# Kernel tuning notes

Hardware: AMD Instinct MI355X
Metric: run time of the kernel (lower is better)

Reference implementation:

```python
import jax, jax.numpy as jnp
import numpy as np

B, S, H, E, V, OOV = 64, 400, 512, 256, 50000, 100

def setup_inputs() -> dict:
    key = jax.random.key(0)
    ks = jax.random.split(key, 32)
    p = lambda i, shape: jax.random.normal(ks[i], shape, jnp.float32) * 0.02
    emb = p(0, (V, E)).at[0].set(0.0)  # padding_idx=0
    return dict(
        summaries_in=jax.random.randint(ks[1], (B,), 1, V),
        h0=jax.random.normal(ks[2], (B, H), jnp.float32),
        c0=jax.random.normal(ks[3], (B, H), jnp.float32),
        encoder_out=jax.random.normal(ks[4], (B, S, 2 * H), jnp.float32),
        encoder_features=jax.random.normal(ks[5], (S * B, 2 * H), jnp.float32),
        encoder_mask=jnp.ones((S, B), jnp.float32),
        context=jax.random.normal(ks[6], (B, 2 * H), jnp.float32),
        coverage=jax.random.uniform(ks[7], (S, B), jnp.float32) * 0.01,
        texts_extended=jax.random.randint(ks[8], (S, B), 0, V + OOV),
        oov_size=OOV,
        emb=emb,
        W_feat=p(10, (2 * H, 2 * H)), b_feat=p(11, (2 * H,)),
        W_cov=p(12, (2 * H,)), b_cov=p(13, (2 * H,)),
        w_att=p(14, (2 * H,)), b_att=p(15, ()),
        W_ih=p(16, (4 * H, E)), W_hh=p(17, (4 * H, H)),
        b_ih=p(18, (4 * H,)), b_hh=p(19, (4 * H,)),
        W_ctx=p(20, (E, 2 * H + E)), b_ctx=p(21, (E,)),
        W_pg=p(22, (4 * H + E,)), b_pg=p(23, ()),
        W_o1=p(24, (H, 3 * H)), b_o1=p(25, (H,)),
        W_o2=p(26, (V, H)), b_o2=p(27, (V,)),
    )


def reference(summaries_in, h0, c0, encoder_out, encoder_features, encoder_mask,
              context, coverage, texts_extended, oov_size, emb,
              W_feat, b_feat, W_cov, b_cov, w_att, b_att,
              W_ih, W_hh, b_ih, b_hh, W_ctx, b_ctx, W_pg, b_pg,
              W_o1, b_o1, W_o2, b_o2):
    # embedding + context projection: [B, 2H+E] -> [B, E]
    x = emb[summaries_in]
    ctx_out = jnp.concatenate([context, x], axis=1) @ W_ctx.T + b_ctx
    # single LSTM step (torch gate order i, f, g, o)
    gates = ctx_out @ W_ih.T + b_ih + h0 @ W_hh.T + b_hh
    i, f, g, o = jnp.split(gates, 4, axis=1)
    c = jax.nn.sigmoid(f) * c0 + jax.nn.sigmoid(i) * jnp.tanh(g)
    h = jax.nn.sigmoid(o) * jnp.tanh(c)
    hidden_out = jnp.concatenate([h, c], axis=1)  # [B, 2H]
    # Bahdanau attention with coverage
    dec_feat = hidden_out @ W_feat.T + b_feat                 # [B, 2H]
    ef = encoder_features.reshape(S, B, 2 * H)                # [S, B, 2H]
    cov_feat = coverage[..., None] * W_cov + b_cov            # Linear(1, 2H)
    e = jnp.tanh(ef + dec_feat[None] + cov_feat) @ w_att + b_att  # [S, B]
    a = jax.nn.softmax(e, axis=0) * encoder_mask
    a = a / jnp.sum(a, axis=0, keepdims=True)                 # renormalize (Normalize(0))
    ctx_new = jnp.einsum('sb,bsd->bd', a, encoder_out)        # [B, 2H]
    coverage_next = coverage + a
    # pointer-generator mix
    gen_in = jnp.concatenate([ctx_new, hidden_out, ctx_out], axis=1)  # [B, 4H+E]
    p_gen = jax.nn.sigmoid(gen_in @ W_pg + b_pg)[:, None]             # [B, 1]
    logits = (jnp.concatenate([h, ctx_new], axis=1) @ W_o1.T + b_o1) @ W_o2.T + b_o2
    vocab_dist = p_gen * jax.nn.softmax(logits, axis=1)       # [B, V]
    attn_w = (1.0 - p_gen) * a.T                              # [B, S]
    vd = jnp.concatenate([vocab_dist, jnp.zeros((B, oov_size), vocab_dist.dtype)], axis=1)
    vd = vd.at[jnp.arange(B)[:, None], texts_extended.T].add(attn_w)  # scatter_add copy dist
    return vd, hidden_out, ctx_new, a, coverage_next
```

## Files before the change

### kernel.cpp

```cpp
#include <hip/hip_runtime.h>
#include <cmath>

#define B 64
#define S 400
#define H 512
#define E 256
#define V 50000
#define OOV 100
#define H2 1024
#define VDN (V + OOV)
#define NBLK_V 782
#define SC 25

typedef __attribute__((ext_vector_type(8))) short short8;
typedef __attribute__((ext_vector_type(4))) float f32x4;

__device__ __forceinline__ float wred_sum(float v) {
#pragma unroll
  for (int o = 32; o > 0; o >>= 1) v += __shfl_down(v, o, 64);
  return v;
}
__device__ __forceinline__ float wred_max(float v) {
#pragma unroll
  for (int o = 32; o > 0; o >>= 1) v = fmaxf(v, __shfl_down(v, o, 64));
  return v;
}
__device__ __forceinline__ short f2bf(float f) {
  return __builtin_bit_cast(short, (__bf16)f);
}
__device__ __forceinline__ float bf2f(unsigned short u) {
  unsigned x = (unsigned)u << 16;
  return __builtin_bit_cast(float, x);
}
__device__ __forceinline__ float ftanh(float x) {
  float e = __expf(2.f * x);
  return 1.f - 2.f * __builtin_amdgcn_rcpf(e + 1.f);
}
__device__ __forceinline__ float fsig(float x) {
  return __builtin_amdgcn_rcpf(1.f + __expf(-x));
}

__global__ __launch_bounds__(256) void k_pre(
    const float* __restrict__ b_ctx, const float* __restrict__ b_ih,
    const float* __restrict__ b_hh, const float* __restrict__ b_feat,
    const float* __restrict__ b_o1, const float* __restrict__ context,
    const float* __restrict__ emb, const int* __restrict__ sumin,
    const float* __restrict__ h0, float* __restrict__ ctxoutT4,
    float* __restrict__ gates, float* __restrict__ dfeat,
    float* __restrict__ innerT4, float* __restrict__ catT4,
    float* __restrict__ h0T4, float* __restrict__ Zb) {
  int idx = blockIdx.x * 256 + threadIdx.x;
  if (idx < 64) Zb[idx] = 0.f;
  if (idx < 16384) {
    int j = ((idx >> 8) << 2) + (idx & 3);
    ctxoutT4[idx] = b_ctx[j];
  } else if (idx < 16384 + 131072) {
    int i = idx - 16384;
    int j = i & 2047;
    gates[i] = b_ih[j] + b_hh[j];
  } else if (idx < 16384 + 131072 + 65536) {
    int i = idx - 16384 - 131072;
    dfeat[i] = b_feat[i & 1023];
  } else if (idx < 245760) {
    int i = idx - 16384 - 131072 - 65536;
    int j = ((i >> 8) << 2) + (i & 3);
    innerT4[i] = b_o1[j];
  } else if (idx < 245760 + 81920) {
    int i = idx - 245760;
    int e = i & 3, b = (i >> 2) & 63, q = i >> 8;
    int k = q * 4 + e;
    catT4[i] = (k < 1024) ? context[b * 1024 + k]
                          : emb[(size_t)sumin[b] * 256 + (k - 1024)];
  } else {
    int i = idx - 245760 - 81920;
    int e = i & 3, b = (i >> 2) & 63, q = i >> 8;
    h0T4[i] = h0[b * 512 + q * 4 + e];
  }
}

template <int R, int KC, int OUTMODE>
__global__ __launch_bounds__(256) void k_gemmsk(
    const float* __restrict__ A1, const float* __restrict__ W1, int ldw1, int s1,
    const float* __restrict__ A2, const float* __restrict__ W2, int ldw2,
    float* __restrict__ out, int ldout) {
  const int lane = threadIdx.x;
  const int w = threadIdx.y;
  const int j0 = blockIdx.x * (4 * R) + w * R;
  const float* A;
  const float* W;
  int ldw, kc0;
  if ((int)blockIdx.y < s1) {
    A = A1; W = W1; ldw = ldw1; kc0 = blockIdx.y * KC;
  } else {
    A = A2; W = W2; ldw = ldw2; kc0 = (blockIdx.y - s1) * KC;
  }
  float acc[R];
#pragma unroll
  for (int r = 0; r < R; ++r) acc[r] = 0.f;
  const float* ap = A + (size_t)kc0 * 256 + lane * 4;
  const float* wr[R];
#pragma unroll
  for (int r = 0; r < R; ++r) wr[r] = W + (size_t)(j0 + r) * ldw + kc0 * 4;
#pragma unroll 8
  for (int k4 = 0; k4 < KC; ++k4) {
    float4 av = *(const float4*)(ap + (size_t)k4 * 256);
#pragma unroll
    for (int r = 0; r < R; ++r) {
      float4 wv = *(const float4*)(wr[r] + k4 * 4);
      acc[r] += av.x * wv.x + av.y * wv.y + av.z * wv.z + av.w * wv.w;
    }
  }
#pragma unroll
  for (int r = 0; r < R; ++r) {
    int j = j0 + r;
    if constexpr (OUTMODE == 0)
      atomicAdd(&out[((size_t)(j >> 2) * 64 + lane) * 4 + (j & 3)], acc[r]);
    else
      atomicAdd(&out[(size_t)lane * ldout + j], acc[r]);
  }
}

__global__ __launch_bounds__(256) void k_lstm(const float* __restrict__ gates,
                                              const float* __restrict__ c0,
                                              float* __restrict__ hidden,
                                              float* __restrict__ hcT4) {
  int idx = blockIdx.x * 256 + threadIdx.x;
  int b = idx >> 9, u = idx & 511;
  float gi = gates[(size_t)b * 2048 + u];
  float gf = gates[(size_t)b * 2048 + 512 + u];
  float gg = gates[(size_t)b * 2048 + 1024 + u];
  float go = gates[(size_t)b * 2048 + 1536 + u];
  float c = fsig(gf) * c0[(size_t)b * 512 + u] + fsig(gi) * ftanh(gg);
  float h = fsig(go) * ftanh(c);
  hidden[(size_t)b * H2 + u] = h;
  hidden[(size_t)b * H2 + 512 + u] = c;
  hcT4[((u >> 2) * 64 + b) * 4 + (u & 3)] = h;
  int k = 512 + u;
  hcT4[((k >> 2) * 64 + b) * 4 + (k & 3)] = c;
}

__global__ __launch_bounds__(256) void k_ectx(
    const float* __restrict__ ef, const float* __restrict__ dfeat,
    const float* __restrict__ cov, const float* __restrict__ Wcov,
    const float* __restrict__ bcov, const float* __restrict__ watt,
    const float* __restrict__ batt, const float* __restrict__ mask,
    const float* __restrict__ enc, float* __restrict__ e_x,
    float* __restrict__ Zb, float* __restrict__ partc) {
  const int t = threadIdx.x;
  const int lane = t & 63;
  const int w = t >> 6;
  const int b = blockIdx.x & 63;
  const int g = blockIdx.x >> 6;
  const int s0 = g * 16 + w * 4;
  __shared__ float s_dbc[1024], s_wc[1024], s_wa[1024];
  for (int i = t; i < 1024; i += 256) {
    s_dbc[i] = dfeat[(size_t)b * H2 + i] + bcov[i];
    s_wc[i] = Wcov[i];
    s_wa[i] = watt[i];
  }
  __syncthreads();

  float4 evs[4][4], ens[4][4];
  float cv[4], mk[4];
#pragma unroll
  for (int r = 0; r < 4; ++r) {
    const int s = s0 + r;
    const float4* efr = (const float4*)(ef + (size_t)(s * B + b) * H2);
    const float4* enr = (const float4*)(enc + ((size_t)b * S + s) * H2);
#pragma unroll
    for (int k = 0; k < 4; ++k) {
      evs[r][k] = efr[k * 64 + lane];
      ens[r][k] = enr[k * 64 + lane];
    }
    cv[r] = cov[s * B + b];
    mk[r] = mask[s * B + b];
  }
  __builtin_amdgcn_sched_barrier(0);

  const float ba = batt[0];
  float x[4];
  float zsum = 0.f;
#pragma unroll
  for (int r = 0; r < 4; ++r) {
    float d = 0.f;
#pragma unroll
    for (int k = 0; k < 4; ++k) {
      const int i4 = (k * 64 + lane) * 4;
      d += ftanh(evs[r][k].x + s_dbc[i4 + 0] + cv[r] * s_wc[i4 + 0]) * s_wa[i4 + 0];
      d += ftanh(evs[r][k].y + s_dbc[i4 + 1] + cv[r] * s_wc[i4 + 1]) * s_wa[i4 + 1];
      d += ftanh(evs[r][k].z + s_dbc[i4 + 2] + cv[r] * s_wc[i4 + 2]) * s_wa[i4 + 2];
      d += ftanh(evs[r][k].w + s_dbc[i4 + 3] + cv[r] * s_wc[i4 + 3]) * s_wa[i4 + 3];
    }
#pragma unroll
    for (int o = 32; o > 0; o >>= 1) d += __shfl_xor(d, o, 64);
    x[r] = mk[r] * __expf(d + ba);
    if (lane == 0) e_x[(s0 + r) * B + b] = x[r];
    zsum += x[r];
  }
  if (lane == 0) atomicAdd(&Zb[b], zsum);
  float4 acc[4];
#pragma unroll
  for (int k = 0; k < 4; ++k) acc[k] = make_float4(0.f, 0.f, 0.f, 0.f);
#pragma unroll
  for (int r = 0; r < 4; ++r) {
#pragma unroll
    for (int k = 0; k < 4; ++k) {
      acc[k].x += x[r] * ens[r][k].x;
      acc[k].y += x[r] * ens[r][k].y;
      acc[k].z += x[r] * ens[r][k].z;
      acc[k].w += x[r] * ens[r][k].w;
    }
  }
  __shared__ float lacc[4][16][64];
#pragma unroll
  for (int k = 0; k < 4; ++k) {
    lacc[w][k * 4 + 0][lane] = acc[k].x;
    lacc[w][k * 4 + 1][lane] = acc[k].y;
    lacc[w][k * 4 + 2][lane] = acc[k].z;
    lacc[w][k * 4 + 3][lane] = acc[k].w;
  }
  __syncthreads();
#pragma unroll
  for (int j = 0; j < 4; ++j) {
    int dim = j * 256 + t;
    int ln = (dim & 255) >> 2, c = dim & 3;
    float ssum = lacc[0][j * 4 + c][ln] + lacc[1][j * 4 + c][ln] +
                 lacc[2][j * 4 + c][ln] + lacc[3][j * 4 + c][ln];
    partc[(size_t)blockIdx.x * H2 + dim] = ssum;
  }
}

__global__ __launch_bounds__(256) void k_ctxpg(
    const float* __restrict__ partc, const float* __restrict__ e_x,
    const float* __restrict__ Zb, const float* __restrict__ coverage,
    const float* __restrict__ hidden, const float* __restrict__ ctxoutT4,
    const float* __restrict__ Wpg, const float* __restrict__ bpg,
    float* __restrict__ ctx_new, float* __restrict__ ctxT4,
    float* __restrict__ pgen, float* __restrict__ a_out,
    float* __restrict__ cov_out) {
  const int b = blockIdx.x;
  const int t = threadIdx.x;
  const int lane = t & 63, w = t >> 6;
  const float rZ = 1.f / Zb[b];
  const int d = t * 4;
  float4 s = make_float4(0.f, 0.f, 0.f, 0.f);
#pragma unroll
  for (int sc = 0; sc < SC; ++sc) {
    float4 v = *(const float4*)(partc + (size_t)(sc * 64 + b) * H2 + d);
    s.x += v.x; s.y += v.y; s.z += v.z; s.w += v.w;
  }
  s.x *= rZ; s.y *= rZ; s.z *= rZ; s.w *= rZ;
  *(float4*)(ctx_new + (size_t)b * H2 + d) = s;
  *(float4*)(ctxT4 + (size_t)t * 256 + b * 4) = s;
#pragma unroll
  for (int i = 0; i < 2; ++i) {
    int sidx = t + i * 256;
    if (sidx < S) {
      int sb = sidx * B + b;
      float av = e_x[sb] * rZ;
      a_out[sb] = av;
      cov_out[sb] = coverage[sb] + av;
    }
  }
  float p = s.x * Wpg[d] + s.y * Wpg[d + 1] + s.z * Wpg[d + 2] + s.w * Wpg[d + 3];
#pragma unroll
  for (int j = 0; j < 4; ++j) {
    int k = t + j * 256;
    p += hidden[(size_t)b * H2 + k] * Wpg[1024 + k];
  }
  p += ctxoutT4[(size_t)(t >> 2) * 256 + b * 4 + (t & 3)] * Wpg[2048 + t];
  p = wred_sum(p);
  __shared__ float red[4];
  if (lane == 0) red[w] = p;
  __syncthreads();
  if (t == 0) {
    float dd = red[0] + red[1] + red[2] + red[3] + bpg[0];
    pgen[b] = fsig(dd);
  }
}

__global__ __launch_bounds__(256) void k_packinner(const float* __restrict__ innerT4,
                                                   short8* __restrict__ packB) {
  int f = blockIdx.x * 256 + threadIdx.x;
  int l = f & 63, bt = (f >> 6) & 3, ks = f >> 8;
  int b = bt * 16 + (l & 15);
  int kbase = ks * 32 + (l >> 4) * 8;
  float4 q0 = *(const float4*)&innerT4[(size_t)(kbase / 4) * 256 + b * 4];
  float4 q1 = *(const float4*)&innerT4[(size_t)(kbase / 4 + 1) * 256 + b * 4];
  short8 frag;
  frag[0] = f2bf(q0.x); frag[1] = f2bf(q0.y);
  frag[2] = f2bf(q0.z); frag[3] = f2bf(q0.w);
  frag[4] = f2bf(q1.x); frag[5] = f2bf(q1.y);
  frag[6] = f2bf(q1.z); frag[7] = f2bf(q1.w);
  packB[f] = frag;
}

__global__ __launch_bounds__(256) void k_mfma_logits(
    const float* __restrict__ W2, const short8* __restrict__ packB,
    const float* __restrict__ bias, unsigned short* __restrict__ logits_bf,
    float* __restrict__ mp, float* __restrict__ zp) {
  const int l = threadIdx.x;
  const int w = threadIdx.y;
  const int jblk = blockIdx.x * 64;
  const int jv = min(jblk + w * 16 + (l & 15), V - 1);
  const float4* wp4 = (const float4*)(W2 + (size_t)jv * 512 + (l >> 4) * 8);

  f32x4 acc0 = {0.f, 0.f, 0.f, 0.f}, acc1 = acc0, acc2 = acc0, acc3 = acc0;
  float4 cw0 = wp4[0], cw1 = wp4[1];
#pragma unroll
  for (int ks = 0; ks < 16; ++ks) {
    float4 nw0, nw1;
    if (ks < 15) { nw0 = wp4[(ks + 1) * 8]; nw1 = wp4[(ks + 1) * 8 + 1]; }
    short8 af;
    af[0] = f2bf(cw0.x); af[1] = f2bf(cw0.y); af[2] = f2bf(cw0.z); af[3] = f2bf(cw0.w);
    af[4] = f2bf(cw1.x); af[5] = f2bf(cw1.y); af[6] = f2bf(cw1.z); af[7] = f2bf(cw1.w);
    short8 b0 = packB[(ks * 4 + 0) * 64 + l];
    short8 b1 = packB[(ks * 4 + 1) * 64 + l];
    short8 b2 = packB[(ks * 4 + 2) * 64 + l];
    short8 b3 = packB[(ks * 4 + 3) * 64 + l];
    acc0 = __builtin_amdgcn_mfma_f32_16x16x32_bf16(af, b0, acc0, 0, 0, 0);
    acc1 = __builtin_amdgcn_mfma_f32_16x16x32_bf16(af, b1, acc1, 0, 0, 0);
    acc2 = __builtin_amdgcn_mfma_f32_16x16x32_bf16(af, b2, acc2, 0, 0, 0);
    acc3 = __builtin_amdgcn_mfma_f32_16x16x32_bf16(af, b3, acc3, 0, 0, 0);
    if (ks < 15) { cw0 = nw0; cw1 = nw1; }
  }

  __shared__ float tile[64][65];
  const int rbase = w * 16 + (l >> 4) * 4;
#pragma unroll
  for (int v = 0; v < 4; ++v) {
    int jl = rbase + v;
    int j = jblk + jl;
    float bv = bias[min(j, V - 1)];
    bool valid = (j < V);
    tile[jl][0 * 16 + (l & 15)] = valid ? acc0[v] + bv : -INFINITY;
    tile[jl][1 * 16 + (l & 15)] = valid ? acc1[v] + bv : -INFINITY;
    tile[jl][2 * 16 + (l & 15)] = valid ? acc2[v] + bv : -INFINITY;
    tile[jl][3 * 16 + (l & 15)] = valid ? acc3[v] + bv : -INFINITY;
  }
  __syncthreads();
  const int t = w * 64 + l;
#pragma unroll
  for (int i = 0; i < 16; ++i) {
    int idx = i * 256 + t;
    int jl = idx & 63;
    int b = idx >> 6;
    int j = jblk + jl;
    if (j < V)
      logits_bf[(size_t)b * V + j] = (unsigned short)f2bf(tile[jl][b]);
  }
  if (t < 64) {
    float m = -INFINITY;
#pragma unroll
    for (int jl = 0; jl < 64; ++jl) m = fmaxf(m, tile[jl][t]);
    float z = 0.f;
#pragma unroll
    for (int jl = 0; jl < 64; ++jl) z += __expf(tile[jl][t] - m);
    mp[(size_t)blockIdx.x * 64 + t] = m;
    zp[(size_t)blockIdx.x * 64 + t] = z;
  }
}

__global__ __launch_bounds__(256) void k_vdms(
    const unsigned short* __restrict__ logits_bf, const float* __restrict__ mp,
    const float* __restrict__ zp, const float* __restrict__ pgen,
    const float* __restrict__ a_out, const int* __restrict__ tex,
    float* __restrict__ out) {
  const int b = blockIdx.x >> 3;
  const int c = blockIdx.x & 7;
  const int t = threadIdx.x;
  const int lane = t & 63, w = t >> 6;
  __shared__ float red[4];
  __shared__ float hist[6272];
  float m = -INFINITY;
  for (int i = t; i < NBLK_V; i += 256) m = fmaxf(m, mp[i * 64 + b]);
  m = wred_max(m);
  if (lane == 0) red[w] = m;
  __syncthreads();
  const float M = fmaxf(fmaxf(red[0], red[1]), fmaxf(red[2], red[3]));
  __syncthreads();
  float z = 0.f;
  for (int i = t; i < NBLK_V; i += 256) z += zp[i * 64 + b] * __expf(mp[i * 64 + b] - M);
  z = wred_sum(z);
  if (lane == 0) red[w] = z;
  __syncthreads();
  const float Z = red[0] + red[1] + red[2] + red[3];
  const float pg = pgen[b];
  const float scale = pg / Z;
  const float wq = 1.f - pg;
  const int v0 = c * 6272;
  const int v1 = min(v0 + 6272, VDN);
  for (int i = t; i < 6272; i += 256) hist[i] = 0.f;
  __syncthreads();
  for (int s = t; s < S; s += 256) {
    int v = tex[s * B + b];
    if (v >= v0 && v < v1) atomicAdd(&hist[v - v0], wq * a_out[s * B + b]);
  }
  __syncthreads();
  for (int v = v0 + t; v < v1; v += 256) {
    float val =
        (v < V) ? scale * __expf(bf2f(logits_bf[(size_t)b * V + v]) - M) : 0.f;
    out[(size_t)b * VDN + v] = val + hist[v - v0];
  }
}

extern "C" void kernel_launch(void* const* d_in, const int* in_sizes, int n_in,
                              void* d_out, int out_size, void* d_ws, size_t ws_size,
                              hipStream_t stream) {
  const int* sumin = (const int*)d_in[0];
  const float* h0 = (const float*)d_in[1];
  const float* c0 = (const float*)d_in[2];
  const float* enc_out = (const float*)d_in[3];
  const float* ef = (const float*)d_in[4];
  const float* mask = (const float*)d_in[5];
  const float* context = (const float*)d_in[6];
  const float* coverage = (const float*)d_in[7];
  const int* tex = (const int*)d_in[8];
  const float* emb = (const float*)d_in[10];
  const float* W_feat = (const float*)d_in[11];
  const float* b_feat = (const float*)d_in[12];
  const float* W_cov = (const float*)d_in[13];
  const float* b_cov = (const float*)d_in[14];
  const float* w_att = (const float*)d_in[15];
  const float* b_att = (const float*)d_in[16];
  const float* W_ih = (const float*)d_in[17];
  const float* W_hh = (const float*)d_in[18];
  const float* b_ih = (const float*)d_in[19];
  const float* b_hh = (const float*)d_in[20];
  const float* W_ctx = (const float*)d_in[21];
  const float* b_ctx = (const float*)d_in[22];
  const float* W_pg = (const float*)d_in[23];
  const float* b_pg = (const float*)d_in[24];
  const float* W_o1 = (const float*)d_in[25];
  const float* b_o1 = (const float*)d_in[26];
  const float* W_o2 = (const float*)d_in[27];
  const float* b_o2 = (const float*)d_in[28];

  float* out = (float*)d_out;
  float* vd = out;
  float* hidden = vd + (size_t)B * VDN;
  float* ctx_new = hidden + (size_t)B * H2;
  float* a_out = ctx_new + (size_t)B * H2;
  float* cov_out = a_out + (size_t)S * B;

  float* ws = (float*)d_ws;
  float* catT4 = ws;
  float* h0T4 = catT4 + 81920;
  float* ctxoutT4 = h0T4 + 32768;
  float* gates = ctxoutT4 + 16384;
  float* hidcatT4 = gates + 131072;
  float* dfeat = hidcatT4 + 65536;
  float* e_x = dfeat + 65536;
  float* ctxnewT4 = e_x + 25600;
  float* innerT4 = ctxnewT4 + 65536;
  float* pgen = innerT4 + 32768;
  float* Zb = pgen + 64;
  float* mp = Zb + 64;
  float* zp = mp + 50048;
  float* packBf = zp + 50048;
  float* logits = packBf + 16384;
  float* partc = logits + 1600064;
  short8* packB = (short8*)packBf;
  unsigned short* logits_bf = (unsigned short*)logits;

  dim3 gblk(64, 4);

  k_pre<<<1408, 256, 0, stream>>>(b_ctx, b_ih, b_hh, b_feat, b_o1, context, emb,
                                  sumin, h0, ctxoutT4, gates, dfeat, innerT4,
                                  catT4, h0T4, Zb);
  k_gemmsk<2, 64, 0><<<dim3(32, 5), gblk, 0, stream>>>(
      catT4, W_ctx, 1280, 5, nullptr, nullptr, 0, ctxoutT4, 0);
  k_gemmsk<2, 64, 1><<<dim3(256, 3), gblk, 0, stream>>>(
      ctxoutT4, W_ih, 256, 1, h0T4, W_hh, 512, gates, 2048);
  k_lstm<<<128, 256, 0, stream>>>(gates, c0, hidden, hidcatT4);
  k_gemmsk<2, 64, 1><<<dim3(128, 4), gblk, 0, stream>>>(
      hidcatT4, W_feat, 1024, 4, nullptr, nullptr, 0, dfeat, 1024);
  k_ectx<<<SC * B, 256, 0, stream>>>(ef, dfeat, coverage, W_cov, b_cov, w_att,
                                     b_att, mask, enc_out, e_x, Zb, partc);
  k_ctxpg<<<B, 256, 0, stream>>>(partc, e_x, Zb, coverage, hidden, ctxoutT4,
                                 W_pg, b_pg, ctx_new, ctxnewT4, pgen, a_out,
                                 cov_out);
  k_gemmsk<2, 64, 0><<<dim3(64, 6), gblk, 0, stream>>>(
      hidcatT4, W_o1, 1536, 2, ctxnewT4, W_o1 + 512, 1536, innerT4, 0);
  k_packinner<<<16, 256, 0, stream>>>(innerT4, packB);
  k_mfma_logits<<<NBLK_V, gblk, 0, stream>>>(W_o2, packB, b_o2, logits_bf, mp, zp);
  k_vdms<<<B * 8, 256, 0, stream>>>(logits_bf, mp, zp, pgen, a_out, tex, vd);
}
```

Before: 218.9 us.

## Double-buffer encoder rows through LDS in attention kernel with per-wave partials

Restructures the attention-score/context kernel so each wave walks 7 consecutive source positions. The encoder_features rows are double-buffered into LDS via global_load_lds while encoder_out rows are prefetched into registers. The cross-wave LDS reduction and block sync at the end are removed: each wave writes its own partial context vector, giving 64 partitions instead of 25. The intent is to overlap loads with the tanh/dot compute and to cut register pressure. In exchange, only two rows are in flight per wave, the partial buffer grows, and the reduction kernel reads more than twice as many partials.

```diff
diff --git a/kernel.cpp b/kernel.cpp
--- a/kernel.cpp
+++ b/kernel.cpp
@@ -10,7 +10,8 @@
 #define H2 1024
 #define VDN (V + OOV)
 #define NBLK_V 782
-#define SC 25
+#define ROWS 7
+#define NPART 64
 
 typedef __attribute__((ext_vector_type(8))) short short8;
 typedef __attribute__((ext_vector_type(4))) float f32x4;
@@ -38,6 +39,11 @@
 }
 __device__ __forceinline__ float fsig(float x) {
   return __builtin_amdgcn_rcpf(1.f + __expf(-x));
+}
+__device__ __forceinline__ void gload_lds16(const float* g, float* l) {
+  __builtin_amdgcn_global_load_lds(
+      (const __attribute__((address_space(1))) unsigned int*)g,
+      (__attribute__((address_space(3))) unsigned int*)l, 16, 0, 0);
 }
 
 __global__ __launch_bounds__(256) void k_pre(
@@ -151,83 +157,88 @@
   const int w = t >> 6;
   const int b = blockIdx.x & 63;
   const int g = blockIdx.x >> 6;
-  const int s0 = g * 16 + w * 4;
-  __shared__ float s_dbc[1024], s_wc[1024], s_wa[1024];
+  const int p = g * 4 + w;
+  __shared__ float inv[3 * 1024];
+  __shared__ float efb[4][2][1024];
   for (int i = t; i < 1024; i += 256) {
-    s_dbc[i] = dfeat[(size_t)b * H2 + i] + bcov[i];
-    s_wc[i] = Wcov[i];
-    s_wa[i] = watt[i];
-  }
-  __syncthreads();
-
-  float4 evs[4][4], ens[4][4];
-  float cv[4], mk[4];
-#pragma unroll
-  for (int r = 0; r < 4; ++r) {
-    const int s = s0 + r;
-    const float4* efr = (const float4*)(ef + (size_t)(s * B + b) * H2);
-    const float4* enr = (const float4*)(enc + ((size_t)b * S + s) * H2);
-#pragma unroll
-    for (int k = 0; k < 4; ++k) {
-      evs[r][k] = efr[k * 64 + lane];
-      ens[r][k] = enr[k * 64 + lane];
+    inv[i] = dfeat[(size_t)b * H2 + i] + bcov[i];
+    inv[1024 + i] = Wcov[i];
+    inv[2048 + i] = watt[i];
+  }
+  __syncthreads();
+  const float ba = batt[0];
+
+  float4 encR[2][4];
+  float cv[2], mk[2];
+  {
+    const int s = min(p * ROWS, S - 1);
+    const float* src = ef + (size_t)(s * B + b) * H2;
+#pragma unroll
+    for (int k = 0; k < 4; ++k)
+      gload_lds16(src + k * 256 + lane * 4, &efb[w][0][k * 256]);
+    const float4* er = (const float4*)(enc + ((size_t)b * S + s) * H2);
+#pragma unroll
+    for (int k = 0; k < 4; ++k) encR[0][k] = er[k * 64 + lane];
+    cv[0] = cov[s * B + b];
+    mk[0] = mask[s * B + b];
+  }
+
+  float4 acc[4];
+#pragma unroll
+  for (int k = 0; k < 4; ++k) acc[k] = make_float4(0.f, 0.f, 0.f, 0.f);
+  float zsum = 0.f;
+
+#pragma unroll
+  for (int i = 0; i < ROWS; ++i) {
+    const int cur = i & 1, nxt = cur ^ 1;
+    asm volatile("s_waitcnt vmcnt(0)" ::: "memory");
+    __builtin_amdgcn_sched_barrier(0);
+    float4 ev[4];
+#pragma unroll
+    for (int k = 0; k < 4; ++k)
+      ev[k] = ((const float4*)&efb[w][cur][0])[k * 64 + lane];
+    __builtin_amdgcn_sched_barrier(0);
+    if (i + 1 < ROWS) {
+      const int s2 = min(p * ROWS + i + 1, S - 1);
+      const float* src = ef + (size_t)(s2 * B + b) * H2;
+#pragma unroll
+      for (int k = 0; k < 4; ++k)
+        gload_lds16(src + k * 256 + lane * 4, &efb[w][nxt][k * 256]);
+      const float4* er = (const float4*)(enc + ((size_t)b * S + s2) * H2);
+#pragma unroll
+      for (int k = 0; k < 4; ++k) encR[nxt][k] = er[k * 64 + lane];
+      cv[nxt] = cov[s2 * B + b];
+      mk[nxt] = mask[s2 * B + b];
     }
-    cv[r] = cov[s * B + b];
-    mk[r] = mask[s * B + b];
-  }
-  __builtin_amdgcn_sched_barrier(0);
-
-  const float ba = batt[0];
-  float x[4];
-  float zsum = 0.f;
-#pragma unroll
-  for (int r = 0; r < 4; ++r) {
+    __builtin_amdgcn_sched_barrier(0);
+    const int s = p * ROWS + i;
+    const bool valid = (s < S);
     float d = 0.f;
 #pragma unroll
     for (int k = 0; k < 4; ++k) {
       const int i4 = (k * 64 + lane) * 4;
-      d += ftanh(evs[r][k].x + s_dbc[i4 + 0] + cv[r] * s_wc[i4 + 0]) * s_wa[i4 + 0];
-      d += ftanh(evs[r][k].y + s_dbc[i4 + 1] + cv[r] * s_wc[i4 + 1]) * s_wa[i4 + 1];
-      d += ftanh(evs[r][k].z + s_dbc[i4 + 2] + cv[r] * s_wc[i4 + 2]) * s_wa[i4 + 2];
-      d += ftanh(evs[r][k].w + s_dbc[i4 + 3] + cv[r] * s_wc[i4 + 3]) * s_wa[i4 + 3];
+      d += ftanh(ev[k].x + inv[i4 + 0] + cv[cur] * inv[1024 + i4 + 0]) * inv[2048 + i4 + 0];
+      d += ftanh(ev[k].y + inv[i4 + 1] + cv[cur] * inv[1024 + i4 + 1]) * inv[2048 + i4 + 1];
+      d += ftanh(ev[k].z + inv[i4 + 2] + cv[cur] * inv[1024 + i4 + 2]) * inv[2048 + i4 + 2];
+      d += ftanh(ev[k].w + inv[i4 + 3] + cv[cur] * inv[1024 + i4 + 3]) * inv[2048 + i4 + 3];
     }
 #pragma unroll
     for (int o = 32; o > 0; o >>= 1) d += __shfl_xor(d, o, 64);
-    x[r] = mk[r] * __expf(d + ba);
-    if (lane == 0) e_x[(s0 + r) * B + b] = x[r];
-    zsum += x[r];
+    float x = valid ? mk[cur] * __expf(d + ba) : 0.f;
+    if (valid && lane == 0) e_x[s * B + b] = x;
+    zsum += x;
+#pragma unroll
+    for (int k = 0; k < 4; ++k) {
+      acc[k].x += x * encR[cur][k].x;
+      acc[k].y += x * encR[cur][k].y;
+      acc[k].z += x * encR[cur][k].z;
+      acc[k].w += x * encR[cur][k].w;
+    }
   }
   if (lane == 0) atomicAdd(&Zb[b], zsum);
-  float4 acc[4];
-#pragma unroll
-  for (int k = 0; k < 4; ++k) acc[k] = make_float4(0.f, 0.f, 0.f, 0.f);
-#pragma unroll
-  for (int r = 0; r < 4; ++r) {
-#pragma unroll
-    for (int k = 0; k < 4; ++k) {
-      acc[k].x += x[r] * ens[r][k].x;
-      acc[k].y += x[r] * ens[r][k].y;
-      acc[k].z += x[r] * ens[r][k].z;
-      acc[k].w += x[r] * ens[r][k].w;
-    }
-  }
-  __shared__ float lacc[4][16][64];
-#pragma unroll
-  for (int k = 0; k < 4; ++k) {
-    lacc[w][k * 4 + 0][lane] = acc[k].x;
-    lacc[w][k * 4 + 1][lane] = acc[k].y;
-    lacc[w][k * 4 + 2][lane] = acc[k].z;
-    lacc[w][k * 4 + 3][lane] = acc[k].w;
-  }
-  __syncthreads();
-#pragma unroll
-  for (int j = 0; j < 4; ++j) {
-    int dim = j * 256 + t;
-    int ln = (dim & 255) >> 2, c = dim & 3;
-    float ssum = lacc[0][j * 4 + c][ln] + lacc[1][j * 4 + c][ln] +
-                 lacc[2][j * 4 + c][ln] + lacc[3][j * 4 + c][ln];
-    partc[(size_t)blockIdx.x * H2 + dim] = ssum;
-  }
+#pragma unroll
+  for (int k = 0; k < 4; ++k)
+    ((float4*)(partc + (size_t)(p * 64 + b) * H2))[k * 64 + lane] = acc[k];
 }
 
 __global__ __launch_bounds__(256) void k_ctxpg(
@@ -244,8 +255,8 @@
   const float rZ = 1.f / Zb[b];
   const int d = t * 4;
   float4 s = make_float4(0.f, 0.f, 0.f, 0.f);
-#pragma unroll
-  for (int sc = 0; sc < SC; ++sc) {
+#pragma unroll 8
+  for (int sc = 0; sc < NPART; ++sc) {
     float4 v = *(const float4*)(partc + (size_t)(sc * 64 + b) * H2 + d);
     s.x += v.x; s.y += v.y; s.z += v.z; s.w += v.w;
   }
@@ -475,8 +486,8 @@
   k_lstm<<<128, 256, 0, stream>>>(gates, c0, hidden, hidcatT4);
   k_gemmsk<2, 64, 1><<<dim3(128, 4), gblk, 0, stream>>>(
       hidcatT4, W_feat, 1024, 4, nullptr, nullptr, 0, dfeat, 1024);
-  k_ectx<<<SC * B, 256, 0, stream>>>(ef, dfeat, coverage, W_cov, b_cov, w_att,
-                                     b_att, mask, enc_out, e_x, Zb, partc);
+  k_ectx<<<16 * 64, 256, 0, stream>>>(ef, dfeat, coverage, W_cov, b_cov, w_att,
+                                      b_att, mask, enc_out, e_x, Zb, partc);
   k_ctxpg<<<B, 256, 0, stream>>>(partc, e_x, Zb, coverage, hidden, ctxoutT4,
                                  W_pg, b_pg, ctx_new, ctxnewT4, pgen, a_out,
                                  cov_out);
```

Result: no change. 220.8 us (+0.9%).
